# Performance work log

Hardware: AMD Instinct MI355X
Metric: run time of the kernel (lower is better)

The kernel has to match this reference:

```python
import jax, jax.numpy as jnp
import numpy as np

N = 256          # Preisach mesh resolution (n)
T = 2000         # number of applied-field time steps
H_MIN, H_MAX = 0.0, 1.0


def setup_inputs() -> dict:
    key = jax.random.key(0)
    k1, = jax.random.split(key, 1)
    h = jax.random.uniform(k1, (T,), dtype=jnp.float32)  # applied field history
    vec_shape = N * (N + 1) // 2  # = n^2/2 + n/2 = 32896
    raw_density = jnp.ones((vec_shape,), dtype=jnp.float32)  # _raw_hyst_density_vector
    offset = jnp.zeros((1,), dtype=jnp.float32)
    scale = jnp.ones((1,), dtype=jnp.float32)
    return {"h": h, "raw_density": raw_density, "offset": offset, "scale": scale}


def reference(h, raw_density, offset, scale):
    dtype = h.dtype
    # asymmetric mesh on [0,1]: alpha (yy) varies along rows, beta (xx) along cols
    x = jnp.linspace(0.0, 1.0, N, dtype=dtype)
    yy = jnp.broadcast_to(x[:, None], (N, N))  # alpha thresholds
    xx = jnp.broadcast_to(x[None, :], (N, N))  # beta thresholds
    tril_mask = jnp.tril(jnp.ones((N, N), dtype=dtype))

    h_norm = (h - H_MIN) / (H_MAX - H_MIN)  # normalize_h
    hs = jnp.concatenate([jnp.full((1,), H_MIN, dtype=dtype), h_norm])

    # initial state: all hysterions off, then tril (matches states[0] of original)
    init_state = -tril_mask

    def step(state, hp):
        h_prev, h_cur = hp
        swept_up = jnp.where(yy >= h_cur, state, 1.0)    # increasing field
        swept_down = jnp.where(xx <= h_cur, state, -1.0) # decreasing field
        new = jnp.where(h_cur > h_prev, swept_up,
                        jnp.where(h_cur < h_prev, swept_down, state))
        new = new * tril_mask  # torch.tril
        return new, new

    # scan over (hs[i-1], hs[i]) pairs -> states[1:] of the original, shape (T, N, N)
    _, states = jax.lax.scan(step, init_state, (hs[:-1], hs[1:]))

    # density: softplus then vector_to_tril (row-major lower-triangular fill)
    dens_vec = jax.nn.softplus(raw_density)
    ii, jj = jnp.tril_indices(N)
    dens = jnp.zeros((N, N), dtype=dtype).at[ii, jj].set(dens_vec)

    tri_size = N * (N + 1) / 2.0  # get_upper_trainagle_size(n)
    b = jnp.einsum('tjk,jk->t', states, dens) / tri_size
    return b * scale[0] + offset[0]
```

## Files before the change

kernel.cpp:

```cpp
#include <hip/hip_runtime.h>
#include <math.h>


#define CL 32
#define GSZ (518 * 64)

__device__ __forceinline__ int make_code(const float* __restrict__ h, int t, int T) {
    const float delta = 1.0f / 255.0f;
    int code = 256;
    if (t < T) {
        const float hc = h[t];
        const float hp = (t == 0) ? 0.0f : h[t - 1];
        if (hc > hp) {
            int i2 = (int)(hc * 255.0f);
            if (i2 > 255) i2 = 255;
            while (i2 < 255 && (float)(i2 + 1) * delta < hc) ++i2;
            while (i2 >= 0 && (float)i2 * delta >= hc) --i2;
            code = ((i2 + 1) << 16) | 256;
        } else if (hc < hp) {
            int kk = (int)(hc * 255.0f);
            if (kk > 255) kk = 255;
            while (kk < 255 && (float)(kk + 1) * delta <= hc) ++kk;
            while (kk > 0 && (float)kk * delta > hc) --kk;
            code = kk;
        }
    }
    return code;
}

__global__ __launch_bounds__(256)
void k1_compose_gbuild(const float* __restrict__ h, const float* __restrict__ raw,
                       int* __restrict__ codes, int2* __restrict__ lohi,
                       float* __restrict__ Gg, int T, int NCH, int NB3) {
    const int b = blockIdx.x;
    const int tid = threadIdx.x;
    const int w = tid >> 6, l = tid & 63;
    if (b < NB3) {
        const int q = b * 4 + w;
        if (q >= NCH) return;
        int mycode = 256;
        if (l < CL) {
            mycode = make_code(h, q * CL + l, T);
            codes[q * CL + l] = mycode;
        }
        int lo[4] = {-1, -1, -1, -1}, hi[4] = {256, 256, 256, 256};
        #pragma unroll
        for (int s = 0; s < CL; ++s) {
            const int cd = __shfl(mycode, s);
            const int k = cd & 0xFFFF, u = cd >> 16;
            #pragma unroll
            for (int j = 0; j < 4; ++j) {
                const int r = j * 64 + l;
                const int rr = (r < u) ? r : -1;
                lo[j] = max(min(lo[j], k), rr);
                hi[j] = max(min(hi[j], k), rr);
            }
        }
        #pragma unroll
        for (int j = 0; j < 4; ++j)
            lohi[q * 256 + j * 64 + l] = make_int2(lo[j], hi[j]);
    } else {
        const int r = (b - NB3) * 4 + w;
        const int tri = r * (r + 1) / 2;
        int lcol, idx0;
        if (r < 64)       { lcol = r;       idx0 = 0; }
        else if (r < 128) { lcol = r - 64;  idx0 = 259; }
        else if (r < 192) { lcol = 191 - r; idx0 = 325 + lcol; }
        else              { lcol = 255 - r; idx0 = lcol + 2; }

        float Pseg[4];
        float carry = 0.0f;
        const int nseg = r / 64 + 1;
        #pragma unroll
        for (int s = 0; s < 4; ++s) {
            Pseg[s] = 0.0f;
            if (s < nseg) {
                const int j = s * 64 + l;
                float v = 0.0f;
                if (j <= r) {
                    const float x = raw[tri + j];
                    v = fmaxf(x, 0.0f) + log1pf(expf(-fabsf(x)));
                }
                #pragma unroll
                for (int off = 1; off < 64; off <<= 1) {
                    const float t2 = __shfl_up(v, off);
                    if (l >= off) v += t2;
                }
                Pseg[s] = carry + v;
                carry += __shfl(v, 63);
            }
        }
        const float tot = carry;
        if (l == 0) Gg[idx0 * 64 + lcol] = -tot;
        #pragma unroll
        for (int s = 0; s < 4; ++s) {
            const int j = s * 64 + l;
            if (j <= r) Gg[(idx0 + 1 + j) * 64 + lcol] = 2.0f * Pseg[s] - tot;
        }
    }
}

__global__ __launch_bounds__(256)
void k3_eval(const int* __restrict__ codes, const int2* __restrict__ lohi,
             const float* __restrict__ Gg,
             const float* __restrict__ scale, const float* __restrict__ offset,
             float* __restrict__ out, int T, int NCH) {
    __shared__ __align__(16) float Gl[GSZ];
    __shared__ __align__(16) int cds[4 * CL];

    const int tid = threadIdx.x;
    const int w = tid >> 6, l = tid & 63;
    const int i = blockIdx.x;
    const int q = i * 4 + w;

    {
        const float4* __restrict__ Gf4 = (const float4*)Gg;
        float4* Gl4 = (float4*)Gl;
        #pragma unroll 4
        for (int j = tid; j < GSZ / 4; j += 256) Gl4[j] = Gf4[j];
    }
    if (tid < 4 * CL) {
        const int gi = i * 4 * CL + tid;
        cds[tid] = (gi < NCH * CL) ? codes[gi] : 256;
    }
    __syncthreads();

    if (q < NCH) {
        const int rows[4] = { l, 64 + l, 191 - l, 255 - l };
        const int base[4] = { 1, 260, 326 + l, l + 3 };
        int c0 = -1, c1 = -1, c2 = -1, c3 = -1;

        #pragma unroll 4
        for (int j = 0; j < q; ++j) {
            const int2 a = lohi[j * 256 + rows[0]];
            const int2 b2 = lohi[j * 256 + rows[1]];
            const int2 cc = lohi[j * 256 + rows[2]];
            const int2 d = lohi[j * 256 + rows[3]];
            c0 = max(min(c0, a.y), a.x);
            c1 = max(min(c1, b2.y), b2.x);
            c2 = max(min(c2, cc.y), cc.x);
            c3 = max(min(c3, d.y), d.x);
        }

        float myout = 0.0f;
        #pragma unroll 4
        for (int s = 0; s < CL; ++s) {
            const int cd = cds[w * CL + s];
            const int k = cd & 0xFFFF, u = cd >> 16;
            c0 = max(min(c0, k), (rows[0] < u) ? rows[0] : -1);
            c1 = max(min(c1, k), (rows[1] < u) ? rows[1] : -1);
            c2 = max(min(c2, k), (rows[2] < u) ? rows[2] : -1);
            c3 = max(min(c3, k), (rows[3] < u) ? rows[3] : -1);
            float p = Gl[(base[0] + c0) * 64 + l] + Gl[(base[1] + c1) * 64 + l]
                    + Gl[(base[2] + c2) * 64 + l] + Gl[(base[3] + c3) * 64 + l];
            #pragma unroll
            for (int off = 32; off; off >>= 1) p += __shfl_xor(p, off);
            if (l == s) myout = p;
        }
        const int t = q * CL + l;
        if (l < CL && t < T)
            out[t] = myout * (1.0f / 32896.0f) * scale[0] + offset[0];
    }
}

extern "C" void kernel_launch(void* const* d_in, const int* in_sizes, int n_in,
                              void* d_out, int out_size, void* d_ws, size_t ws_size,
                              hipStream_t stream) {
    const float* h      = (const float*)d_in[0];
    const float* raw    = (const float*)d_in[1];
    const float* offset = (const float*)d_in[2];
    const float* scale  = (const float*)d_in[3];
    float* out = (float*)d_out;
    const int T = in_sizes[0];
    const int NCH = (T + CL - 1) / CL;
    const int NB3 = (NCH + 3) / 4;

    char* ws = (char*)d_ws;
    size_t o = 0;
    int* codes = (int*)(ws + o);  o += ((size_t)NCH * CL * 4 + 15) & ~15ull;
    int2* lohi = (int2*)(ws + o); o += (size_t)NCH * 256 * 8;
    float* Gg  = (float*)(ws + o);

    k1_compose_gbuild<<<NB3 + 64, 256, 0, stream>>>(h, raw, codes, lohi, Gg, T, NCH, NB3);
    k3_eval<<<NB3, 256, 0, stream>>>(codes, lohi, Gg, scale, offset, out, T, NCH);
}
```

Measured before the change: 81.36 us.

## Split eval kernel into one block per chunk with one row per thread

The eval kernel now launches one block per 32-step chunk instead of one per four chunks. Each thread owns a single mesh row rather than four, and the four wavefronts' partial sums are combined through shared memory before the output is written. The serial prefix composition over earlier chunks' lohi entries now issues one dependent load per iteration per thread instead of four, and it runs before the barrier, so it overlaps with the shared-memory fill of the G table. In exchange, each of the four times as many blocks reloads the full ~132KB G table into shared memory, and an extra barrier is added.

Measured after the change: 75.70 us. -7.0%, faster.

```diff
diff --git a/kernel.cpp b/kernel.cpp
--- a/kernel.cpp
+++ b/kernel.cpp
@@ -31,11 +31,11 @@
 __global__ __launch_bounds__(256)
 void k1_compose_gbuild(const float* __restrict__ h, const float* __restrict__ raw,
                        int* __restrict__ codes, int2* __restrict__ lohi,
-                       float* __restrict__ Gg, int T, int NCH, int NB3) {
+                       float* __restrict__ Gg, int T, int NCH, int NB1) {
     const int b = blockIdx.x;
     const int tid = threadIdx.x;
     const int w = tid >> 6, l = tid & 63;
-    if (b < NB3) {
+    if (b < NB1) {
         const int q = b * 4 + w;
         if (q >= NCH) return;
         int mycode = 256;
@@ -60,7 +60,7 @@
         for (int j = 0; j < 4; ++j)
             lohi[q * 256 + j * 64 + l] = make_int2(lo[j], hi[j]);
     } else {
-        const int r = (b - NB3) * 4 + w;
+        const int r = (b - NB1) * 4 + w;
         const int tri = r * (r + 1) / 2;
         int lcol, idx0;
         if (r < 64)       { lcol = r;       idx0 = 0; }
@@ -106,12 +106,13 @@
              const float* __restrict__ scale, const float* __restrict__ offset,
              float* __restrict__ out, int T, int NCH) {
     __shared__ __align__(16) float Gl[GSZ];
-    __shared__ __align__(16) int cds[4 * CL];
+    __shared__ int cds[CL];
+    __shared__ float cb[4 * CL];
 
     const int tid = threadIdx.x;
     const int w = tid >> 6, l = tid & 63;
-    const int i = blockIdx.x;
-    const int q = i * 4 + w;
+    const int q = blockIdx.x;
+    const int r = tid;
 
     {
         const float4* __restrict__ Gf4 = (const float4*)Gg;
@@ -119,47 +120,41 @@
         #pragma unroll 4
         for (int j = tid; j < GSZ / 4; j += 256) Gl4[j] = Gf4[j];
     }
-    if (tid < 4 * CL) {
-        const int gi = i * 4 * CL + tid;
-        cds[tid] = (gi < NCH * CL) ? codes[gi] : 256;
+    if (tid < CL) cds[tid] = codes[q * CL + tid];
+
+    int c = -1;
+    #pragma unroll 4
+    for (int j = 0; j < q; ++j) {
+        const int2 lh = lohi[j * 256 + r];
+        c = max(min(c, lh.y), lh.x);
     }
     __syncthreads();
 
-    if (q < NCH) {
-        const int rows[4] = { l, 64 + l, 191 - l, 255 - l };
-        const int base[4] = { 1, 260, 326 + l, l + 3 };
-        int c0 = -1, c1 = -1, c2 = -1, c3 = -1;
+    int gbase, lcol;
+    if (w == 0)      { gbase = 1;        lcol = l; }
+    else if (w == 1) { gbase = 260;      lcol = l; }
+    else if (w == 2) { gbase = 389 - l;  lcol = 63 - l; }
+    else             { gbase = 66 - l;   lcol = 63 - l; }
 
-        #pragma unroll 4
-        for (int j = 0; j < q; ++j) {
-            const int2 a = lohi[j * 256 + rows[0]];
-            const int2 b2 = lohi[j * 256 + rows[1]];
-            const int2 cc = lohi[j * 256 + rows[2]];
-            const int2 d = lohi[j * 256 + rows[3]];
-            c0 = max(min(c0, a.y), a.x);
-            c1 = max(min(c1, b2.y), b2.x);
-            c2 = max(min(c2, cc.y), cc.x);
-            c3 = max(min(c3, d.y), d.x);
+    float myout = 0.0f;
+    #pragma unroll 4
+    for (int s = 0; s < CL; ++s) {
+        const int cd = cds[s];
+        const int k = cd & 0xFFFF, u = cd >> 16;
+        c = max(min(c, k), (r < u) ? r : -1);
+        float p = Gl[(gbase + c) * 64 + lcol];
+        #pragma unroll
+        for (int off = 32; off; off >>= 1) p += __shfl_xor(p, off);
+        if (l == s) myout = p;
+    }
+    if (l < CL) cb[w * CL + l] = myout;
+    __syncthreads();
+    if (w == 0 && l < CL) {
+        const int t = q * CL + l;
+        if (t < T) {
+            const float sum = cb[l] + cb[CL + l] + cb[2 * CL + l] + cb[3 * CL + l];
+            out[t] = sum * (1.0f / 32896.0f) * scale[0] + offset[0];
         }
-
-        float myout = 0.0f;
-        #pragma unroll 4
-        for (int s = 0; s < CL; ++s) {
-            const int cd = cds[w * CL + s];
-            const int k = cd & 0xFFFF, u = cd >> 16;
-            c0 = max(min(c0, k), (rows[0] < u) ? rows[0] : -1);
-            c1 = max(min(c1, k), (rows[1] < u) ? rows[1] : -1);
-            c2 = max(min(c2, k), (rows[2] < u) ? rows[2] : -1);
-            c3 = max(min(c3, k), (rows[3] < u) ? rows[3] : -1);
-            float p = Gl[(base[0] + c0) * 64 + l] + Gl[(base[1] + c1) * 64 + l]
-                    + Gl[(base[2] + c2) * 64 + l] + Gl[(base[3] + c3) * 64 + l];
-            #pragma unroll
-            for (int off = 32; off; off >>= 1) p += __shfl_xor(p, off);
-            if (l == s) myout = p;
-        }
-        const int t = q * CL + l;
-        if (l < CL && t < T)
-            out[t] = myout * (1.0f / 32896.0f) * scale[0] + offset[0];
     }
 }
 
@@ -173,7 +168,7 @@
     float* out = (float*)d_out;
     const int T = in_sizes[0];
     const int NCH = (T + CL - 1) / CL;
-    const int NB3 = (NCH + 3) / 4;
+    const int NB1 = (NCH + 3) / 4;
 
     char* ws = (char*)d_ws;
     size_t o = 0;
@@ -181,6 +176,6 @@
     int2* lohi = (int2*)(ws + o); o += (size_t)NCH * 256 * 8;
     float* Gg  = (float*)(ws + o);
 
-    k1_compose_gbuild<<<NB3 + 64, 256, 0, stream>>>(h, raw, codes, lohi, Gg, T, NCH, NB3);
-    k3_eval<<<NB3, 256, 0, stream>>>(codes, lohi, Gg, scale, offset, out, T, NCH);
+    k1_compose_gbuild<<<NB1 + 64, 256, 0, stream>>>(h, raw, codes, lohi, Gg, T, NCH, NB1);
+    k3_eval<<<NCH, 256, 0, stream>>>(codes, lohi, Gg, scale, offset, out, T, NCH);
 }
```
